# Kernel optimization log

Hardware: AMD Instinct MI355X
Metric: run time of the kernel (lower is better)

## Reference

```python
import jax, jax.numpy as jnp
import numpy as np


def _gcn_conv(x, W, b, src, dst, norm, n_nodes):
    # PyG GCNConv: h = x @ W, then symmetric-normalized aggregation, then + b
    h = x @ W                                   # [N, F_out]
    msg = h[src] * norm[:, None]                # gather + scale, [E', F_out]
    agg = jax.ops.segment_sum(msg, dst, num_segments=n_nodes)
    return agg + b


def _norm_and_loops(edge_index, n_nodes):
    # add self-loops, compute D^{-1/2} (A+I) D^{-1/2} edge weights
    loop = jnp.arange(n_nodes, dtype=edge_index.dtype)
    src = jnp.concatenate([edge_index[0], loop])
    dst = jnp.concatenate([edge_index[1], loop])
    deg = jax.ops.segment_sum(jnp.ones_like(dst, dtype=jnp.float32), dst,
                              num_segments=n_nodes)
    dinv = jnp.where(deg > 0, jax.lax.rsqrt(deg), 0.0)
    norm = dinv[src] * dinv[dst]
    return src, dst, norm


def setup_inputs() -> dict:
    key = jax.random.key(0)
    ks = jax.random.split(key, 4)
    N, E, n_latent, n_dim = 50000, 800000, 128, 128
    hidden = 2 * n_latent
    x = jax.random.normal(ks[0], (N, n_latent), dtype=jnp.float32)
    edge_index = jax.random.randint(ks[1], (2, E), 0, N, dtype=jnp.int64)
    W1 = jax.random.normal(ks[2], (n_latent, hidden), dtype=jnp.float32) / np.sqrt(n_latent)
    b1 = jnp.zeros((hidden,), dtype=jnp.float32)
    W2 = jax.random.normal(ks[3], (hidden, n_dim), dtype=jnp.float32) / np.sqrt(hidden)
    b2 = jnp.zeros((n_dim,), dtype=jnp.float32)
    return {"x": x, "edge_index": edge_index, "W1": W1, "b1": b1,
            "W2": W2, "b2": b2}


def reference(x, edge_index, W1, b1, W2, b2):
    n_nodes = x.shape[0]
    src, dst, norm = _norm_and_loops(edge_index, n_nodes)
    z1 = jax.nn.relu(_gcn_conv(x, W1, b1, src, dst, norm, n_nodes))
    z2 = _gcn_conv(z1, W2, b2, src, dst, norm, n_nodes)
    return z2
```

## Files before the change

### kernel.cpp

```cpp
#include <hip/hip_runtime.h>


constexpr int F = 128;
constexpr int HID = 256;
constexpr int ECHUNK = 8192;

typedef __attribute__((ext_vector_type(8))) _Float16 f16x8;
typedef __attribute__((ext_vector_type(4))) _Float16 f16x4;
typedef __attribute__((ext_vector_type(4))) float f32x4;

__global__ __launch_bounds__(256) void k_prep(const int* __restrict__ dst,
                                              unsigned* __restrict__ bhist,
                                              const float* __restrict__ W1,
                                              const float* __restrict__ W2,
                                              const float* __restrict__ x,
                                              _Float16* __restrict__ w1t,
                                              _Float16* __restrict__ w2t,
                                              _Float16* __restrict__ xh,
                                              int E, int nbC, int n4) {
  __shared__ unsigned hist[256];
  int b = blockIdx.x;
  int tid = threadIdx.x;
  if (b < nbC) {
    hist[tid] = 0u;
    __syncthreads();
    int i0 = b * ECHUNK;
    int i1 = min(i0 + ECHUNK, E);
    for (int i = i0 + tid; i < i1; i += 256)
      atomicAdd(&hist[((unsigned)dst[i]) >> 8], 1u);
    __syncthreads();
    bhist[b * 256 + tid] = hist[tid];
  } else if (b < nbC + 128) {
    int idx = (b - nbC) * 256 + tid;
    int k = idx / HID, n = idx - k * HID;
    w1t[n * F + k] = (_Float16)W1[idx];
  } else if (b < nbC + 256) {
    int idx = (b - nbC - 128) * 256 + tid;
    int k = idx / F, n = idx - k * F;
    w2t[n * HID + k] = (_Float16)W2[idx];
  } else {
    int i = (b - nbC - 256) * 256 + tid;
    if (i < n4) {
      float4 v = ((const float4*)x)[i];
      f16x4 o;
      o.x = (_Float16)v.x; o.y = (_Float16)v.y;
      o.z = (_Float16)v.z; o.w = (_Float16)v.w;
      ((f16x4*)xh)[i] = o;
    }
  }
}

__global__ __launch_bounds__(256) void k_bscan(const unsigned* __restrict__ bhist,
                                               int nbC,
                                               unsigned* __restrict__ bbase,
                                               unsigned* __restrict__ bcur,
                                               int* __restrict__ rowptr,
                                               int P, int N, int E) {
  __shared__ unsigned wsum[4];
  int tid = threadIdx.x;
  unsigned v = 0u;
  for (int c = 0; c < nbC; ++c) v += bhist[c * 256 + tid];
  if (tid >= P) v = 0u;
  unsigned sv = v;
#pragma unroll
  for (int off = 1; off < 64; off <<= 1) {
    unsigned t = __shfl_up(sv, off);
    if ((tid & 63) >= off) sv += t;
  }
  int w = tid >> 6;
  if ((tid & 63) == 63) wsum[w] = sv;
  __syncthreads();
  unsigned wpre = 0;
  for (int k = 0; k < w; ++k) wpre += wsum[k];
  unsigned excl = wpre + sv - v;
  if (tid < P) {
    bbase[tid] = excl;
    bcur[tid] = excl;
  }
  if (tid == P - 1) bbase[P] = excl + v;
  if (tid == 0) rowptr[N] = E;
}

__global__ __launch_bounds__(256) void k_binscat(const int* __restrict__ src,
                                                 const int* __restrict__ dst,
                                                 const unsigned* __restrict__ bhist,
                                                 unsigned* __restrict__ bcur,
                                                 unsigned* __restrict__ packed, int E) {
  __shared__ unsigned hist[256];
  __shared__ unsigned basel[256];
  int tid = threadIdx.x;
  unsigned c = bhist[blockIdx.x * 256 + tid];
  if (c) basel[tid] = atomicAdd(&bcur[tid], c);
  hist[tid] = 0u;
  __syncthreads();
  int i0 = blockIdx.x * ECHUNK;
  int i1 = min(i0 + ECHUNK, E);
  for (int i = i0 + tid; i < i1; i += 256) {
    unsigned d = (unsigned)dst[i];
    unsigned b = d >> 8;
    unsigned pos = basel[b] + atomicAdd(&hist[b], 1u);
    packed[pos] = ((unsigned)src[i]) | ((d & 255u) << 16);
  }
}

__global__ __launch_bounds__(256) void k_bcsr(const unsigned* __restrict__ packed,
                                              const unsigned* __restrict__ bbase,
                                              float* __restrict__ dinv,
                                              int* __restrict__ rowptr,
                                              unsigned short* __restrict__ esrc,
                                              int N) {
  __shared__ unsigned hist[256];
  __shared__ unsigned rowloc[256];
  __shared__ unsigned cur[256];
  __shared__ unsigned wsum[4];
  int tid = threadIdx.x, b = blockIdx.x;
  int e0 = (int)bbase[b], e1 = (int)bbase[b + 1];
  hist[tid] = 0u;
  __syncthreads();
  for (int i = e0 + tid; i < e1; i += 256)
    atomicAdd(&hist[packed[i] >> 16], 1u);
  __syncthreads();
  unsigned v = hist[tid];
  unsigned sv = v;
#pragma unroll
  for (int off = 1; off < 64; off <<= 1) {
    unsigned t = __shfl_up(sv, off);
    if ((tid & 63) >= off) sv += t;
  }
  int w = tid >> 6;
  if ((tid & 63) == 63) wsum[w] = sv;
  __syncthreads();
  unsigned wpre = 0;
  for (int k = 0; k < w; ++k) wpre += wsum[k];
  unsigned excl = wpre + sv - v;
  int node = b * 256 + tid;
  if (node < N) {
    dinv[node] = rsqrtf((float)v + 1.0f);
    rowptr[node] = e0 + (int)excl;
  }
  rowloc[tid] = (unsigned)e0 + excl;
  cur[tid] = 0u;
  __syncthreads();
  for (int i = e0 + tid; i < e1; i += 256) {
    unsigned pk = packed[i];
    unsigned dl = pk >> 16;
    unsigned pos = rowloc[dl] + atomicAdd(&cur[dl], 1u);
    esrc[pos] = (unsigned short)(pk & 0xffffu);
  }
}

__global__ __launch_bounds__(256) void k_agg1(const int* __restrict__ rowptr,
                                              const unsigned short* __restrict__ esrc,
                                              const float* __restrict__ dinv,
                                              const _Float16* __restrict__ xh,
                                              _Float16* __restrict__ outp, int N) {
  int node = blockIdx.x * 16 + (threadIdx.x >> 4);
  int li = threadIdx.x & 15;
  int lanebase = (threadIdx.x & 63) & 48;
  if (node >= N) return;
  float di = dinv[node];
  float w0 = di * di;
  f16x8 svv = ((const f16x8*)(xh + (size_t)node * F))[li];
  float acc[8] = {};
  int beg = rowptr[node], end = rowptr[node + 1];
  for (int b = beg; b < end; b += 16) {
    int n = min(16, end - b);
    int s = 0;
    float w = 0.f;
    if (li < n) {
      s = (int)esrc[b + li];
      w = dinv[s] * di;
    }
    int t = 0;
    for (; t + 7 < n; t += 8) {
      int ss[8];
      float wz[8];
#pragma unroll
      for (int j = 0; j < 8; ++j) {
        ss[j] = __shfl(s, lanebase + t + j);
        wz[j] = __shfl(w, lanebase + t + j);
      }
      f16x8 vv[8];
#pragma unroll
      for (int j = 0; j < 8; ++j)
        vv[j] = ((const f16x8*)(xh + (size_t)ss[j] * F))[li];
#pragma unroll
      for (int j = 0; j < 8; ++j)
#pragma unroll
        for (int k = 0; k < 8; ++k)
          acc[k] += (float)vv[j][k] * wz[j];
    }
    for (; t + 3 < n; t += 4) {
      int ss[4];
      float wz[4];
#pragma unroll
      for (int j = 0; j < 4; ++j) {
        ss[j] = __shfl(s, lanebase + t + j);
        wz[j] = __shfl(w, lanebase + t + j);
      }
      f16x8 vv[4];
#pragma unroll
      for (int j = 0; j < 4; ++j)
        vv[j] = ((const f16x8*)(xh + (size_t)ss[j] * F))[li];
#pragma unroll
      for (int j = 0; j < 4; ++j)
#pragma unroll
        for (int k = 0; k < 8; ++k)
          acc[k] += (float)vv[j][k] * wz[j];
    }
    for (; t < n; ++t) {
      int s0 = __shfl(s, lanebase + t);
      float wa = __shfl(w, lanebase + t);
      f16x8 v0 = ((const f16x8*)(xh + (size_t)s0 * F))[li];
#pragma unroll
      for (int k = 0; k < 8; ++k) acc[k] += (float)v0[k] * wa;
    }
  }
  f16x8 ov;
#pragma unroll
  for (int k = 0; k < 8; ++k) ov[k] = (_Float16)(acc[k] + (float)svv[k] * w0);
  ((f16x8*)(outp + (size_t)node * F))[li] = ov;
}

__global__ __launch_bounds__(256) void k_agg_out(const int* __restrict__ rowptr,
                                                 const unsigned short* __restrict__ esrc,
                                                 const float* __restrict__ dinv,
                                                 const _Float16* __restrict__ hb,
                                                 const float* __restrict__ bias,
                                                 float* __restrict__ outp, int N) {
  int node = blockIdx.x * 16 + (threadIdx.x >> 4);
  int li = threadIdx.x & 15;
  int lanebase = (threadIdx.x & 63) & 48;
  if (node >= N) return;
  float di = dinv[node];
  float w0 = di * di;
  f16x8 svv = ((const f16x8*)(hb + (size_t)node * F))[li];
  float acc[8] = {};
  int beg = rowptr[node], end = rowptr[node + 1];
  for (int b = beg; b < end; b += 16) {
    int n = min(16, end - b);
    int s = 0;
    float w = 0.f;
    if (li < n) {
      s = (int)esrc[b + li];
      w = dinv[s] * di;
    }
    int t = 0;
    for (; t + 7 < n; t += 8) {
      int ss[8];
      float wz[8];
#pragma unroll
      for (int j = 0; j < 8; ++j) {
        ss[j] = __shfl(s, lanebase + t + j);
        wz[j] = __shfl(w, lanebase + t + j);
      }
      f16x8 vv[8];
#pragma unroll
      for (int j = 0; j < 8; ++j)
        vv[j] = ((const f16x8*)(hb + (size_t)ss[j] * F))[li];
#pragma unroll
      for (int j = 0; j < 8; ++j)
#pragma unroll
        for (int k = 0; k < 8; ++k)
          acc[k] += (float)vv[j][k] * wz[j];
    }
    for (; t + 3 < n; t += 4) {
      int ss[4];
      float wz[4];
#pragma unroll
      for (int j = 0; j < 4; ++j) {
        ss[j] = __shfl(s, lanebase + t + j);
        wz[j] = __shfl(w, lanebase + t + j);
      }
      f16x8 vv[4];
#pragma unroll
      for (int j = 0; j < 4; ++j)
        vv[j] = ((const f16x8*)(hb + (size_t)ss[j] * F))[li];
#pragma unroll
      for (int j = 0; j < 4; ++j)
#pragma unroll
        for (int k = 0; k < 8; ++k)
          acc[k] += (float)vv[j][k] * wz[j];
    }
    for (; t < n; ++t) {
      int s0 = __shfl(s, lanebase + t);
      float wa = __shfl(w, lanebase + t);
      f16x8 v0 = ((const f16x8*)(hb + (size_t)s0 * F))[li];
#pragma unroll
      for (int k = 0; k < 8; ++k) acc[k] += (float)v0[k] * wa;
    }
  }
  float4 bb0 = ((const float4*)bias)[li * 2];
  float4 bb1 = ((const float4*)bias)[li * 2 + 1];
  float4 o0, o1;
  o0.x = acc[0] + (float)svv[0] * w0 + bb0.x;
  o0.y = acc[1] + (float)svv[1] * w0 + bb0.y;
  o0.z = acc[2] + (float)svv[2] * w0 + bb0.z;
  o0.w = acc[3] + (float)svv[3] * w0 + bb0.w;
  o1.x = acc[4] + (float)svv[4] * w0 + bb1.x;
  o1.y = acc[5] + (float)svv[5] * w0 + bb1.y;
  o1.z = acc[6] + (float)svv[6] * w0 + bb1.z;
  o1.w = acc[7] + (float)svv[7] * w0 + bb1.w;
  float* orow = outp + (size_t)node * F + li * 8;
  *(float4*)orow = o0;
  *(float4*)(orow + 4) = o1;
}

__global__ __launch_bounds__(256) void k_fgemm(const _Float16* __restrict__ A,
                                               const _Float16* __restrict__ B1,
                                               const float* __restrict__ bias,
                                               const _Float16* __restrict__ B2,
                                               _Float16* __restrict__ H2, int M) {
  __shared__ _Float16 AL[64 * 128];
  __shared__ _Float16 ZL[64 * 256];
  int tid = threadIdx.x;
  int lane = tid & 63, wid = tid >> 6;
  int row0 = blockIdx.x * 64;

#pragma unroll
  for (int i = 0; i < 4; ++i) {
    int g = i * 256 + tid;
    int r = g >> 4, gi = g & 15;
    int o = r * 128 + ((gi ^ (r & 7)) * 8);
    size_t go = (size_t)(row0 + r) * 128 + gi * 8;
    *(f16x8*)&AL[o] = *(const f16x8*)&A[go];
  }
  __syncthreads();

  f32x4 acc[4][4] = {};
#pragma unroll
  for (int ks = 0; ks < 4; ++ks) {
    f16x8 ah[4], bh[4];
#pragma unroll
    for (int mf = 0; mf < 4; ++mf) {
      int r = mf * 16 + (lane & 15);
      int g = ks * 4 + (lane >> 4);
      ah[mf] = *(const f16x8*)&AL[r * 128 + ((g ^ (r & 7)) * 8)];
    }
#pragma unroll
    for (int nf = 0; nf < 4; ++nf) {
      int c = wid * 64 + nf * 16 + (lane & 15);
      bh[nf] = *(const f16x8*)&B1[(size_t)c * 128 + ks * 32 + (lane >> 4) * 8];
    }
#pragma unroll
    for (int mf = 0; mf < 4; ++mf)
#pragma unroll
      for (int nf = 0; nf < 4; ++nf)
        acc[mf][nf] = __builtin_amdgcn_mfma_f32_16x16x32_f16(
            ah[mf], bh[nf], acc[mf][nf], 0, 0, 0);
  }

#pragma unroll
  for (int mf = 0; mf < 4; ++mf) {
    int r0l = mf * 16 + (lane >> 4) * 4;
#pragma unroll
    for (int nf = 0; nf < 4; ++nf) {
      int c = wid * 64 + nf * 16 + (lane & 15);
      float bv = bias[c];
      int gi = c >> 3, ci = c & 7;
#pragma unroll
      for (int r = 0; r < 4; ++r) {
        int rr = r0l + r;
        float v = fmaxf(acc[mf][nf][r] + bv, 0.f);
        ZL[rr * 256 + ((gi ^ (rr & 7)) * 8) + ci] = (_Float16)v;
      }
    }
  }
  __syncthreads();

  f32x4 acc2[4][2] = {};
#pragma unroll
  for (int ks = 0; ks < 8; ++ks) {
    f16x8 ah[4], bh[2];
#pragma unroll
    for (int mf = 0; mf < 4; ++mf) {
      int r = mf * 16 + (lane & 15);
      int g = ks * 4 + (lane >> 4);
      ah[mf] = *(const f16x8*)&ZL[r * 256 + ((g ^ (r & 7)) * 8)];
    }
#pragma unroll
    for (int nf = 0; nf < 2; ++nf) {
      int c = wid * 32 + nf * 16 + (lane & 15);
      bh[nf] = *(const f16x8*)&B2[(size_t)c * 256 + ks * 32 + (lane >> 4) * 8];
    }
#pragma unroll
    for (int mf = 0; mf < 4; ++mf)
#pragma unroll
      for (int nf = 0; nf < 2; ++nf)
        acc2[mf][nf] = __builtin_amdgcn_mfma_f32_16x16x32_f16(
            ah[mf], bh[nf], acc2[mf][nf], 0, 0, 0);
  }

#pragma unroll
  for (int mf = 0; mf < 4; ++mf) {
    int r0 = row0 + mf * 16 + (lane >> 4) * 4;
#pragma unroll
    for (int nf = 0; nf < 2; ++nf) {
      int c = wid * 32 + nf * 16 + (lane & 15);
#pragma unroll
      for (int r = 0; r < 4; ++r)
        H2[(size_t)(r0 + r) * F + c] = (_Float16)acc2[mf][nf][r];
    }
  }
}

extern "C" void kernel_launch(void* const* d_in, const int* in_sizes, int n_in,
                              void* d_out, int out_size, void* d_ws, size_t ws_size,
                              hipStream_t stream) {
  const float* x = (const float*)d_in[0];
  const int* ei = (const int*)d_in[1];
  const float* W1 = (const float*)d_in[2];
  const float* b1 = (const float*)d_in[3];
  const float* W2 = (const float*)d_in[4];
  const float* b2 = (const float*)d_in[5];
  float* out = (float*)d_out;

  int N = in_sizes[0] / F;
  int E = in_sizes[1] / 2;
  const int* src = ei;
  const int* dst = ei + E;
  int P = (N + 255) / 256;
  int nbC = (E + ECHUNK - 1) / ECHUNK;

  char* ws = (char*)d_ws;
  size_t off = 0;
  auto allocB = [&](size_t bytes) {
    void* p = ws + off;
    off += ((bytes + 255) & ~(size_t)255);
    return p;
  };
  float* dinv = (float*)allocB((size_t)N * 4);
  int* rowptr = (int*)allocB(((size_t)N + 1) * 4);
  unsigned* bbase = (unsigned*)allocB(257 * 4);
  unsigned* bcur = (unsigned*)allocB(256 * 4);
  unsigned* bhist = (unsigned*)allocB((size_t)nbC * 256 * 4);
  unsigned* packed = (unsigned*)allocB((size_t)E * 4);
  unsigned short* esrc = (unsigned short*)allocB((size_t)E * 2);
  _Float16* xh = (_Float16*)allocB((size_t)N * F * 2);
  _Float16* agg = (_Float16*)allocB((size_t)(N + 64) * F * 2);
  _Float16* w1t = (_Float16*)allocB((size_t)F * HID * 2);
  _Float16* w2t = (_Float16*)allocB((size_t)HID * F * 2);
  _Float16* h2 = agg;

  int n4 = N * F / 4;
  int nbPrep = nbC + 256 + (n4 + 255) / 256;

  k_prep<<<nbPrep, 256, 0, stream>>>(dst, bhist, W1, W2, x, w1t, w2t, xh,
                                     E, nbC, n4);
  k_bscan<<<1, 256, 0, stream>>>(bhist, nbC, bbase, bcur, rowptr, P, N, E);
  k_binscat<<<nbC, 256, 0, stream>>>(src, dst, bhist, bcur, packed, E);
  k_bcsr<<<P, 256, 0, stream>>>(packed, bbase, dinv, rowptr, esrc, N);

  int nbAgg = (N + 15) / 16;
  int mb = (N + 63) / 64;

  k_agg1<<<nbAgg, 256, 0, stream>>>(rowptr, esrc, dinv, xh, agg, N);
  k_fgemm<<<mb, 256, 0, stream>>>(agg, w1t, b1, w2t, h2, N);
  k_agg_out<<<nbAgg, 256, 0, stream>>>(rowptr, esrc, dinv, h2, b2, out, N);
}
```

Before: 158.9 us.

## Split feature tables into 32-column planes for cache-friendly gather aggregation

Stores the fp16 feature tables (input x and the second-layer GEMM output) as four column planes of 32 halves each. The aggregation kernels become a single templated kernel with a 2D grid, where blockIdx.y picks the plane and 8 lanes gather 64-byte rows per node. Each plane is 50k×64B (~3.2MB), so the random neighbour gathers should hit L2/MALL more often. In exchange, every edge's index and weight are read and shuffled four times, and each gather becomes a smaller 8-byte-per-lane load.

```diff
diff --git a/kernel.cpp b/kernel.cpp
--- a/kernel.cpp
+++ b/kernel.cpp
@@ -16,7 +16,8 @@
                                               const float* __restrict__ x,
                                               _Float16* __restrict__ w1t,
                                               _Float16* __restrict__ w2t,
-                                              _Float16* __restrict__ xh,
+                                              _Float16* __restrict__ xq,
+                                              size_t pstride,
                                               int E, int nbC, int n4) {
   __shared__ unsigned hist[256];
   int b = blockIdx.x;
@@ -42,10 +43,14 @@
     int i = (b - nbC - 256) * 256 + tid;
     if (i < n4) {
       float4 v = ((const float4*)x)[i];
+      int nd = i >> 5;
+      int c4 = (i & 31) * 4;
+      int plane = c4 >> 5;
+      int incol = c4 & 31;
       f16x4 o;
       o.x = (_Float16)v.x; o.y = (_Float16)v.y;
       o.z = (_Float16)v.z; o.w = (_Float16)v.w;
-      ((f16x4*)xh)[i] = o;
+      *(f16x4*)&xq[(size_t)plane * pstride + (size_t)nd * 32 + incol] = o;
     }
   }
 }
@@ -149,168 +154,84 @@
   }
 }
 
-__global__ __launch_bounds__(256) void k_agg1(const int* __restrict__ rowptr,
+template <int OUTF>
+__global__ __launch_bounds__(256) void k_aggq(const int* __restrict__ rowptr,
                                               const unsigned short* __restrict__ esrc,
                                               const float* __restrict__ dinv,
-                                              const _Float16* __restrict__ xh,
-                                              _Float16* __restrict__ outp, int N) {
-  int node = blockIdx.x * 16 + (threadIdx.x >> 4);
-  int li = threadIdx.x & 15;
-  int lanebase = (threadIdx.x & 63) & 48;
+                                              const _Float16* __restrict__ tblq,
+                                              size_t pstride,
+                                              _Float16* __restrict__ outq,
+                                              const float* __restrict__ bias,
+                                              float* __restrict__ outf, int N) {
+  int q = blockIdx.y;
+  const _Float16* tbl = tblq + (size_t)q * pstride;
+  int node = blockIdx.x * 32 + (threadIdx.x >> 3);
+  int li = threadIdx.x & 7;
+  int lanebase = (threadIdx.x & 63) & 56;
   if (node >= N) return;
   float di = dinv[node];
   float w0 = di * di;
-  f16x8 svv = ((const f16x8*)(xh + (size_t)node * F))[li];
-  float acc[8] = {};
+  f16x4 svv = ((const f16x4*)(tbl + (size_t)node * 32))[li];
+  float acc[4] = {};
   int beg = rowptr[node], end = rowptr[node + 1];
-  for (int b = beg; b < end; b += 16) {
-    int n = min(16, end - b);
+  for (int b = beg; b < end; b += 8) {
+    int n = min(8, end - b);
     int s = 0;
     float w = 0.f;
     if (li < n) {
       s = (int)esrc[b + li];
       w = dinv[s] * di;
     }
-    int t = 0;
-    for (; t + 7 < n; t += 8) {
+    if (n == 8) {
       int ss[8];
       float wz[8];
 #pragma unroll
       for (int j = 0; j < 8; ++j) {
-        ss[j] = __shfl(s, lanebase + t + j);
-        wz[j] = __shfl(w, lanebase + t + j);
+        ss[j] = __shfl(s, lanebase + j);
+        wz[j] = __shfl(w, lanebase + j);
       }
-      f16x8 vv[8];
+      f16x4 vv[8];
 #pragma unroll
       for (int j = 0; j < 8; ++j)
-        vv[j] = ((const f16x8*)(xh + (size_t)ss[j] * F))[li];
+        vv[j] = ((const f16x4*)(tbl + (size_t)ss[j] * 32))[li];
 #pragma unroll
       for (int j = 0; j < 8; ++j)
 #pragma unroll
-        for (int k = 0; k < 8; ++k)
+        for (int k = 0; k < 4; ++k)
           acc[k] += (float)vv[j][k] * wz[j];
-    }
-    for (; t + 3 < n; t += 4) {
-      int ss[4];
-      float wz[4];
-#pragma unroll
-      for (int j = 0; j < 4; ++j) {
-        ss[j] = __shfl(s, lanebase + t + j);
-        wz[j] = __shfl(w, lanebase + t + j);
+    } else {
+      for (int t = 0; t < n; ++t) {
+        int s0 = __shfl(s, lanebase + t);
+        float wa = __shfl(w, lanebase + t);
+        f16x4 v0 = ((const f16x4*)(tbl + (size_t)s0 * 32))[li];
+#pragma unroll
+        for (int k = 0; k < 4; ++k) acc[k] += (float)v0[k] * wa;
       }
-      f16x8 vv[4];
-#pragma unroll
-      for (int j = 0; j < 4; ++j)
-        vv[j] = ((const f16x8*)(xh + (size_t)ss[j] * F))[li];
-#pragma unroll
-      for (int j = 0; j < 4; ++j)
-#pragma unroll
-        for (int k = 0; k < 8; ++k)
-          acc[k] += (float)vv[j][k] * wz[j];
-    }
-    for (; t < n; ++t) {
-      int s0 = __shfl(s, lanebase + t);
-      float wa = __shfl(w, lanebase + t);
-      f16x8 v0 = ((const f16x8*)(xh + (size_t)s0 * F))[li];
-#pragma unroll
-      for (int k = 0; k < 8; ++k) acc[k] += (float)v0[k] * wa;
-    }
-  }
-  f16x8 ov;
-#pragma unroll
-  for (int k = 0; k < 8; ++k) ov[k] = (_Float16)(acc[k] + (float)svv[k] * w0);
-  ((f16x8*)(outp + (size_t)node * F))[li] = ov;
-}
-
-__global__ __launch_bounds__(256) void k_agg_out(const int* __restrict__ rowptr,
-                                                 const unsigned short* __restrict__ esrc,
-                                                 const float* __restrict__ dinv,
-                                                 const _Float16* __restrict__ hb,
-                                                 const float* __restrict__ bias,
-                                                 float* __restrict__ outp, int N) {
-  int node = blockIdx.x * 16 + (threadIdx.x >> 4);
-  int li = threadIdx.x & 15;
-  int lanebase = (threadIdx.x & 63) & 48;
-  if (node >= N) return;
-  float di = dinv[node];
-  float w0 = di * di;
-  f16x8 svv = ((const f16x8*)(hb + (size_t)node * F))[li];
-  float acc[8] = {};
-  int beg = rowptr[node], end = rowptr[node + 1];
-  for (int b = beg; b < end; b += 16) {
-    int n = min(16, end - b);
-    int s = 0;
-    float w = 0.f;
-    if (li < n) {
-      s = (int)esrc[b + li];
-      w = dinv[s] * di;
-    }
-    int t = 0;
-    for (; t + 7 < n; t += 8) {
-      int ss[8];
-      float wz[8];
-#pragma unroll
-      for (int j = 0; j < 8; ++j) {
-        ss[j] = __shfl(s, lanebase + t + j);
-        wz[j] = __shfl(w, lanebase + t + j);
-      }
-      f16x8 vv[8];
-#pragma unroll
-      for (int j = 0; j < 8; ++j)
-        vv[j] = ((const f16x8*)(hb + (size_t)ss[j] * F))[li];
-#pragma unroll
-      for (int j = 0; j < 8; ++j)
-#pragma unroll
-        for (int k = 0; k < 8; ++k)
-          acc[k] += (float)vv[j][k] * wz[j];
-    }
-    for (; t + 3 < n; t += 4) {
-      int ss[4];
-      float wz[4];
-#pragma unroll
-      for (int j = 0; j < 4; ++j) {
-        ss[j] = __shfl(s, lanebase + t + j);
-        wz[j] = __shfl(w, lanebase + t + j);
-      }
-      f16x8 vv[4];
-#pragma unroll
-      for (int j = 0; j < 4; ++j)
-        vv[j] = ((const f16x8*)(hb + (size_t)ss[j] * F))[li];
-#pragma unroll
-      for (int j = 0; j < 4; ++j)
-#pragma unroll
-        for (int k = 0; k < 8; ++k)
-          acc[k] += (float)vv[j][k] * wz[j];
-    }
-    for (; t < n; ++t) {
-      int s0 = __shfl(s, lanebase + t);
-      float wa = __shfl(w, lanebase + t);
-      f16x8 v0 = ((const f16x8*)(hb + (size_t)s0 * F))[li];
-#pragma unroll
-      for (int k = 0; k < 8; ++k) acc[k] += (float)v0[k] * wa;
-    }
-  }
-  float4 bb0 = ((const float4*)bias)[li * 2];
-  float4 bb1 = ((const float4*)bias)[li * 2 + 1];
-  float4 o0, o1;
-  o0.x = acc[0] + (float)svv[0] * w0 + bb0.x;
-  o0.y = acc[1] + (float)svv[1] * w0 + bb0.y;
-  o0.z = acc[2] + (float)svv[2] * w0 + bb0.z;
-  o0.w = acc[3] + (float)svv[3] * w0 + bb0.w;
-  o1.x = acc[4] + (float)svv[4] * w0 + bb1.x;
-  o1.y = acc[5] + (float)svv[5] * w0 + bb1.y;
-  o1.z = acc[6] + (float)svv[6] * w0 + bb1.z;
-  o1.w = acc[7] + (float)svv[7] * w0 + bb1.w;
-  float* orow = outp + (size_t)node * F + li * 8;
-  *(float4*)orow = o0;
-  *(float4*)(orow + 4) = o1;
-}
-
-__global__ __launch_bounds__(256) void k_fgemm(const _Float16* __restrict__ A,
+    }
+  }
+  if (OUTF == 0) {
+    f16x4 ov;
+#pragma unroll
+    for (int k = 0; k < 4; ++k)
+      ov[k] = (_Float16)(acc[k] + (float)svv[k] * w0);
+    ((f16x4*)(outq + (size_t)q * pstride + (size_t)node * 32))[li] = ov;
+  } else {
+    float4 bb = ((const float4*)(bias + q * 32))[li];
+    float4 o;
+    o.x = acc[0] + (float)svv[0] * w0 + bb.x;
+    o.y = acc[1] + (float)svv[1] * w0 + bb.y;
+    o.z = acc[2] + (float)svv[2] * w0 + bb.z;
+    o.w = acc[3] + (float)svv[3] * w0 + bb.w;
+    *(float4*)(outf + (size_t)node * F + q * 32 + li * 4) = o;
+  }
+}
+
+__global__ __launch_bounds__(256) void k_fgemm(const _Float16* __restrict__ Aq,
+                                               size_t pstride,
                                                const _Float16* __restrict__ B1,
                                                const float* __restrict__ bias,
                                                const _Float16* __restrict__ B2,
-                                               _Float16* __restrict__ H2, int M) {
+                                               _Float16* __restrict__ H2q, int M) {
   __shared__ _Float16 AL[64 * 128];
   __shared__ _Float16 ZL[64 * 256];
   int tid = threadIdx.x;
@@ -322,8 +243,10 @@
     int g = i * 256 + tid;
     int r = g >> 4, gi = g & 15;
     int o = r * 128 + ((gi ^ (r & 7)) * 8);
-    size_t go = (size_t)(row0 + r) * 128 + gi * 8;
-    *(f16x8*)&AL[o] = *(const f16x8*)&A[go];
+    int plane = gi >> 2;
+    int incol = (gi & 3) * 8;
+    *(f16x8*)&AL[o] = *(const f16x8*)&Aq[(size_t)plane * pstride +
+                                         (size_t)(row0 + r) * 32 + incol];
   }
   __syncthreads();
 
@@ -396,10 +319,11 @@
     int r0 = row0 + mf * 16 + (lane >> 4) * 4;
 #pragma unroll
     for (int nf = 0; nf < 2; ++nf) {
-      int c = wid * 32 + nf * 16 + (lane & 15);
+      int ic = nf * 16 + (lane & 15);
 #pragma unroll
       for (int r = 0; r < 4; ++r)
-        H2[(size_t)(r0 + r) * F + c] = (_Float16)acc2[mf][nf][r];
+        H2q[(size_t)wid * pstride + (size_t)(r0 + r) * 32 + ic] =
+            (_Float16)acc2[mf][nf][r];
     }
   }
 }
@@ -421,6 +345,8 @@
   const int* dst = ei + E;
   int P = (N + 255) / 256;
   int nbC = (E + ECHUNK - 1) / ECHUNK;
+  int N64 = (N + 63) & ~63;
+  size_t pstride = (size_t)N64 * 32;
 
   char* ws = (char*)d_ws;
   size_t off = 0;
@@ -436,25 +362,27 @@
   unsigned* bhist = (unsigned*)allocB((size_t)nbC * 256 * 4);
   unsigned* packed = (unsigned*)allocB((size_t)E * 4);
   unsigned short* esrc = (unsigned short*)allocB((size_t)E * 2);
-  _Float16* xh = (_Float16*)allocB((size_t)N * F * 2);
-  _Float16* agg = (_Float16*)allocB((size_t)(N + 64) * F * 2);
+  _Float16* xq = (_Float16*)allocB(4 * pstride * 2);
+  _Float16* aggq = (_Float16*)allocB(4 * pstride * 2);
   _Float16* w1t = (_Float16*)allocB((size_t)F * HID * 2);
   _Float16* w2t = (_Float16*)allocB((size_t)HID * F * 2);
-  _Float16* h2 = agg;
+  _Float16* h2q = aggq;
 
   int n4 = N * F / 4;
   int nbPrep = nbC + 256 + (n4 + 255) / 256;
 
-  k_prep<<<nbPrep, 256, 0, stream>>>(dst, bhist, W1, W2, x, w1t, w2t, xh,
-                                     E, nbC, n4);
+  k_prep<<<nbPrep, 256, 0, stream>>>(dst, bhist, W1, W2, x, w1t, w2t, xq,
+                                     pstride, E, nbC, n4);
   k_bscan<<<1, 256, 0, stream>>>(bhist, nbC, bbase, bcur, rowptr, P, N, E);
   k_binscat<<<nbC, 256, 0, stream>>>(src, dst, bhist, bcur, packed, E);
   k_bcsr<<<P, 256, 0, stream>>>(packed, bbase, dinv, rowptr, esrc, N);
 
-  int nbAgg = (N + 15) / 16;
+  dim3 gAgg((N + 31) / 32, 4);
   int mb = (N + 63) / 64;
 
-  k_agg1<<<nbAgg, 256, 0, stream>>>(rowptr, esrc, dinv, xh, agg, N);
-  k_fgemm<<<mb, 256, 0, stream>>>(agg, w1t, b1, w2t, h2, N);
-  k_agg_out<<<nbAgg, 256, 0, stream>>>(rowptr, esrc, dinv, h2, b2, out, N);
-}
+  k_aggq<0><<<gAgg, 256, 0, stream>>>(rowptr, esrc, dinv, xq, pstride,
+                                      aggq, nullptr, nullptr, N);
+  k_fgemm<<<mb, 256, 0, stream>>>(aggq, pstride, w1t, b1, w2t, h2q, N);
+  k_aggq<1><<<gAgg, 256, 0, stream>>>(rowptr, esrc, dinv, h2q, pstride,
+                                      nullptr, b2, out, N);
+}
```

Measured after the change: 190.3 us. +19.8%, slower.
